# Kernel optimization log

Measured on AMD Instinct MI355X. Metric: run time of the kernel, lower is better.

## Reference

```python
import jax, jax.numpy as jnp
import numpy as np

EPS = 1e-12  # F.normalize default eps


def _l2norm(x):
    n = jnp.linalg.norm(x, axis=-1, keepdims=True)
    return x / jnp.maximum(n, EPS)


def setup_inputs() -> dict:
    key = jax.random.key(0)
    k1, k2, k3, k4 = jax.random.split(key, 4)
    N, Tq, Ts, S, D = 16, 1369, 5476, 4, 768
    return {
        "x_query": jax.random.normal(k1, (N, Tq, D), dtype=jnp.float32),
        "x_support": jax.random.normal(k2, (N, Ts, D), dtype=jnp.float32),
        "x_support_cls": jax.random.normal(k3, (N, S, D), dtype=jnp.float32),
        "W_head": jax.random.normal(k4, (3 * D, 1), dtype=jnp.float32) * 0.02,
        "b_head": jnp.zeros((1,), dtype=jnp.float32),
    }


def reference(x_query, x_support, x_support_cls, W_head, b_head):
    N, Tq, D = x_query.shape
    side = int(np.sqrt(Tq))  # token grid side, 37 for 1369 tokens

    # mean CLS over shots, then L2-normalize everything
    cls = _l2norm(jnp.mean(x_support_cls, axis=1, keepdims=True))  # [N,1,D]
    q = _l2norm(x_query)     # [N,Tq,D]
    s = _l2norm(x_support)   # [N,Ts,D]

    # cosine distance matrix and nearest-support reduction
    cd = 1.0 - jnp.einsum("nqd,nsd->nqs", q, s)      # [N,Tq,Ts]
    dmin = jnp.min(cd, axis=-1)                        # [N,Tq]
    idx = jnp.argmin(cd, axis=-1)                      # [N,Tq]
    nearest = jnp.take_along_axis(s, idx[..., None], axis=1)  # [N,Tq,D]

    # head on concat([q, nearest, cls]) -> sigmoid
    feat = jnp.concatenate(
        [q, nearest, jnp.broadcast_to(cls, (N, Tq, D))], axis=-1
    )  # [N,Tq,3D]
    logits = feat @ W_head + b_head                    # [N,Tq,1]
    pred = jax.nn.sigmoid(logits)

    dmin = dmin.reshape(N, 1, side, side)
    pred = pred.reshape(N, 1, side, side)
    return pred * dmin, pred
```

## Files before the change

kernel.cpp:

```cpp
#include <hip/hip_runtime.h>
#include <stdint.h>

#define NB 16
#define TQ 1369
#define TS 5476
#define DD 768

#define BM 128
#define BN 128
#define KB 24
#define RBQ 11
#define RBS 43
#define QPAD 1408
#define SPAD 5504
#define NROWS (NB * QPAD)
#define CAP 8
#define EPS_SEL 2.5e-3f

typedef float f32x4 __attribute__((ext_vector_type(4)));
typedef short short8 __attribute__((ext_vector_type(8)));
typedef unsigned short ushort;
typedef unsigned long long ull;


__device__ inline float waveReduceSum(float v) {
    #pragma unroll
    for (int m = 32; m >= 1; m >>= 1) v += __shfl_xor(v, m);
    return v;
}

__device__ inline unsigned bf16rne(float x) {
    unsigned u = __float_as_uint(x);
    return (u + 0x7FFFu + ((u >> 16) & 1u)) >> 16;
}
__device__ inline unsigned pack2(float lo, float hi) {
    return bf16rne(lo) | (bf16rne(hi) << 16);
}

__device__ inline f32x4 mfma16(short8 a, short8 b, f32x4 c) {
    return __builtin_amdgcn_mfma_f32_16x16x32_bf16(a, b, c, 0, 0, 0);
}

__device__ inline void async16(const void* g, void* l) {
    __builtin_amdgcn_global_load_lds(
        (const __attribute__((address_space(1))) unsigned*)g,
        (__attribute__((address_space(3))) unsigned*)l, 16, 0, 0);
}

__device__ inline unsigned fsort(float f) {
    unsigned u = __float_as_uint(f);
    return (u & 0x80000000u) ? ~u : (u | 0x80000000u);
}
__device__ inline float funsort(unsigned u) {
    return __uint_as_float((u & 0x80000000u) ? (u & 0x7FFFFFFFu) : ~u);
}


__global__ __launch_bounds__(256) void cls_kernel(const float* __restrict__ xc,
                                                  float* __restrict__ cls) {
    int n = blockIdx.x, tid = threadIdx.x;
    const float* base = xc + (size_t)n * 4 * DD;
    float v[3]; float ss = 0.f;
    #pragma unroll
    for (int i = 0; i < 3; i++) {
        int e = tid + i * 256;
        float a = base[e] + base[DD + e] + base[2 * DD + e] + base[3 * DD + e];
        v[i] = a * 0.25f; ss += v[i] * v[i];
    }
    ss = waveReduceSum(ss);
    __shared__ float red[4]; __shared__ float rn;
    if ((tid & 63) == 0) red[tid >> 6] = ss;
    __syncthreads();
    if (tid == 0) {
        float t = red[0] + red[1] + red[2] + red[3];
        rn = 1.0f / fmaxf(sqrtf(t), 1e-12f);
    }
    __syncthreads();
    float r = rn;
    #pragma unroll
    for (int i = 0; i < 3; i++) cls[(size_t)n * DD + tid + i * 256] = v[i] * r;
}


__global__ __launch_bounds__(256) void split_kernel(const float* __restrict__ Q,
                                                    const float* __restrict__ S,
                                                    ushort* __restrict__ Qh,
                                                    ushort* __restrict__ Sh,
                                                    float* __restrict__ rq,
                                                    float* __restrict__ rs) {
    int wid = (int)((blockIdx.x * 256u + threadIdx.x) >> 6);
    int lane = threadIdx.x & 63;
    bool isQ = wid < NB * QPAD;
    int n, row, nreal;
    if (isQ) { n = wid / QPAD; row = wid % QPAD; nreal = TQ; }
    else     { int w2 = wid - NB * QPAD; n = w2 / SPAD; row = w2 % SPAD; nreal = TS; }
    int rb = row >> 7, p = row & 127;
    size_t tbase = isQ ? (size_t)(n * RBQ + rb) * KB * 4096
                       : (size_t)(n * RBS + rb) * KB * 4096;
    ushort* outp = (isQ ? Qh : Sh) + tbase;

    if (row >= nreal) {
        uint4 z = {0u, 0u, 0u, 0u};
        for (int t = lane; t < 96; t += 64) {
            int kb = t >> 2, g = t & 3;
            *(uint4*)(outp + (size_t)kb * 4096 + g * 1024 + p * 8) = z;
        }
        return;
    }

    const float* src = isQ ? Q + ((size_t)n * TQ + row) * DD
                           : S + ((size_t)n * TS + row) * DD;
    float4 x[3]; float ss = 0.f;
    #pragma unroll
    for (int i = 0; i < 3; i++) {
        x[i] = ((const float4*)src)[lane + i * 64];
        ss += x[i].x * x[i].x + x[i].y * x[i].y + x[i].z * x[i].z + x[i].w * x[i].w;
    }
    ss = waveReduceSum(ss);
    float r = 1.0f / fmaxf(sqrtf(ss), 1e-12f);
    if (lane == 0) {
        if (isQ) rq[(size_t)n * TQ + row] = r; else rs[(size_t)n * TS + row] = r;
    }
    #pragma unroll
    for (int i = 0; i < 3; i++) {
        float ax = x[i].x * r, ay = x[i].y * r, az = x[i].z * r, aw = x[i].w * r;
        int k0 = lane * 4 + i * 256;
        int kb = k0 >> 5;
        int g  = (k0 >> 3) & 3;
        int sub = k0 & 7;
        uint2 hv;
        hv.x = pack2(ax, ay);
        hv.y = pack2(az, aw);
        *(uint2*)(outp + (size_t)kb * 4096 + g * 1024 + p * 8 + sub) = hv;
    }
}


__global__ __launch_bounds__(256, 4) void gemm_sel(const ushort* __restrict__ Qh,
                                                   const ushort* __restrict__ Sh,
                                                   float2* __restrict__ hdr,
                                                   uint2* __restrict__ cpair) {
    __shared__ __align__(16) ushort As[4096];
    __shared__ __align__(16) ushort Bs[4096];
    __shared__ ull key[128];
    __shared__ int cnt[128];
    __shared__ uint2 cand[128][CAP];

    int tid = threadIdx.x, w = tid >> 6, lane = tid & 63;
    int bx = blockIdx.x, by = blockIdx.y, n = blockIdx.z;
    int wm = w & 1, wn = w >> 1, g4 = lane >> 4, c16 = lane & 15;

    if (tid < 128) { key[tid] = 0ull; cnt[tid] = 1; }
    __syncthreads();

    const char* gsrc = (const char*)((w < 2)
        ? (Qh + (size_t)(n * RBQ + bx) * KB * 4096)
        : (Sh + (size_t)(n * RBS + by) * KB * 4096)) + wm * 4096 + lane * 16;
    char* lbase = (char*)((w < 2) ? As : Bs) + wm * 4096;

    f32x4 acc[4][4] = {};
    int aoff = g4 * 1024 + wm * 512 + c16 * 8;
    int boff = g4 * 1024 + wn * 512 + c16 * 8;

    for (int kb = 0; kb < KB; kb++) {
        #pragma unroll
        for (int j = 0; j < 4; j++)
            async16(gsrc + (size_t)kb * 8192 + j * 1024, lbase + j * 1024);
        __syncthreads();

        short8 ah[4], bh[4];
        #pragma unroll
        for (int i = 0; i < 4; i++) {
            ah[i] = *(const short8*)&As[aoff + i * 128];
            bh[i] = *(const short8*)&Bs[boff + i * 128];
        }
        #pragma unroll
        for (int mi = 0; mi < 4; mi++)
            #pragma unroll
            for (int ni = 0; ni < 4; ni++)
                acc[mi][ni] = mfma16(ah[mi], bh[ni], acc[mi][ni]);
        __syncthreads();
    }

    int colb = by * 128 + wn * 64 + c16;
    bool edge = (by == RBS - 1);

    #pragma unroll
    for (int mi = 0; mi < 4; mi++) {
        #pragma unroll
        for (int r = 0; r < 4; r++) {
            float v = -1e30f; int c = 0;
            #pragma unroll
            for (int ni = 0; ni < 4; ni++) {
                float d = acc[mi][ni][r];
                int col = colb + ni * 16;
                if ((!edge || col < TS) && d > v) { v = d; c = col; }
            }
            #pragma unroll
            for (int m = 1; m < 16; m <<= 1) {
                float ov = __shfl_xor(v, m);
                int   oc = __shfl_xor(c, m);
                if (ov > v || (ov == v && oc < c)) { v = ov; c = oc; }
            }
            if (c16 == 0) {
                int row = wm * 64 + mi * 16 + g4 * 4 + r;
                ull k = ((ull)fsort(v) << 32) | (unsigned)(8191 - c);
                atomicMax(&key[row], k);
            }
        }
    }
    __syncthreads();

    #pragma unroll
    for (int mi = 0; mi < 4; mi++) {
        #pragma unroll
        for (int r = 0; r < 4; r++) {
            int row = wm * 64 + mi * 16 + g4 * 4 + r;
            ull k = key[row];
            float mx = funsort((unsigned)(k >> 32));
            int amc = 8191 - (int)(k & 0xFFFFFFFFull);
            float thr = mx - EPS_SEL;
            #pragma unroll
            for (int ni = 0; ni < 4; ni++) {
                float d = acc[mi][ni][r];
                int col = colb + ni * 16;
                if ((!edge || col < TS) && d >= thr && col != amc) {
                    int slot = atomicAdd(&cnt[row], 1);
                    if (slot < CAP) {
                        uint2 pr; pr.x = (unsigned)col; pr.y = __float_as_uint(d);
                        cand[row][slot] = pr;
                    }
                }
            }
        }
    }
    __syncthreads();

    if (tid < 128) {
        ull k = key[tid];
        float mx = funsort((unsigned)(k >> 32));
        int amc = 8191 - (int)(k & 0xFFFFFFFFull);
        int cn = min(cnt[tid], CAP);
        size_t rowg = (size_t)n * QPAD + (size_t)bx * 128 + tid;
        size_t rec = (size_t)by * NROWS + rowg;
        hdr[rec] = make_float2(mx, __int_as_float(cn));
        uint2 a0; a0.x = (unsigned)amc; a0.y = __float_as_uint(mx);
        cpair[rec * CAP] = a0;
        for (int i = 1; i < cn; i++) cpair[rec * CAP + i] = cand[tid][i];
    }
}


__global__ __launch_bounds__(256) void merge_head(const float2* __restrict__ hdr,
                                                  const uint2* __restrict__ cpair,
                                                  const float* __restrict__ Q,
                                                  const float* __restrict__ S,
                                                  const float* __restrict__ rq,
                                                  const float* __restrict__ rs,
                                                  const float* __restrict__ cls,
                                                  const float* __restrict__ W,
                                                  const float* __restrict__ bb,
                                                  float* __restrict__ out) {
    int w = threadIdx.x >> 6, lane = threadIdx.x & 63;
    int qi = blockIdx.x * 4 + w;
    int n = qi / TQ, qr = qi - n * TQ;
    size_t rowg = (size_t)n * QPAD + qr;

    float mx_l = -1e30f; int cnt_l = 0;
    if (lane < RBS) {
        float2 h = hdr[(size_t)lane * NROWS + rowg];
        mx_l = h.x; cnt_l = __float_as_int(h.y);
    }
    float gm = mx_l;
    #pragma unroll
    for (int m = 32; m >= 1; m >>= 1) gm = fmaxf(gm, __shfl_xor(gm, m));
    float thr = gm - EPS_SEL;

    const float* qrow = Q + (size_t)qi * DD;
    float4 q4[3];
    #pragma unroll
    for (int i = 0; i < 3; i++) q4[i] = ((const float4*)qrow)[lane + i * 64];
    float rqv = rq[qi];

    float bestd = -1e30f; int bidx = 0x7FFFFFFF;

    auto recheck = [&](int sidx) {
        const float* srow = S + ((size_t)n * TS + sidx) * DD;
        float part = 0.f;
        #pragma unroll
        for (int k = 0; k < 3; k++) {
            float4 s4 = ((const float4*)srow)[lane + k * 64];
            part += q4[k].x * s4.x + q4[k].y * s4.y + q4[k].z * s4.z + q4[k].w * s4.w;
        }
        part = waveReduceSum(part);
        float dot = part * rqv * rs[(size_t)n * TS + sidx];
        if (dot > bestd || (dot == bestd && sidx < bidx)) { bestd = dot; bidx = sidx; }
    };

    ull ball = __ballot(lane < RBS && mx_l >= thr);
    while (ball) {
        int src = __ffsll((long long)ball) - 1;
        ball &= ball - 1;
        int cn = __shfl(cnt_l, src);
        size_t rec = (size_t)src * NROWS + rowg;
        for (int i = 0; i < cn; i++) {
            uint2 pr = cpair[rec * CAP + i];
            float ad = __uint_as_float(pr.y);
            if (ad >= thr) recheck((int)pr.x);
        }
    }
    if (bidx == 0x7FFFFFFF) bidx = 0;
    float dmin = 1.0f - bestd;

    const float* srow = S + ((size_t)n * TS + bidx) * DD;
    const float* clsr = cls + (size_t)n * DD;
    float rsv = rs[(size_t)n * TS + bidx];
    float aq = 0.f, as_ = 0.f, ac = 0.f;
    #pragma unroll
    for (int i = 0; i < 3; i++) {
        float4 s4 = ((const float4*)srow)[lane + i * 64];
        float4 c4 = ((const float4*)clsr)[lane + i * 64];
        float4 w0 = ((const float4*)W)[lane + i * 64];
        float4 w1 = ((const float4*)(W + DD))[lane + i * 64];
        float4 w2 = ((const float4*)(W + 2 * DD))[lane + i * 64];
        aq += q4[i].x * w0.x + q4[i].y * w0.y + q4[i].z * w0.z + q4[i].w * w0.w;
        as_ += s4.x * w1.x + s4.y * w1.y + s4.z * w1.z + s4.w * w1.w;
        ac += c4.x * w2.x + c4.y * w2.y + c4.z * w2.z + c4.w * w2.w;
    }
    float tot = waveReduceSum(aq * rqv + as_ * rsv + ac);
    if (lane == 0) {
        float logit = tot + bb[0];
        float pred = 1.0f / (1.0f + expf(-logit));
        out[qi] = pred * dmin;
        out[NB * TQ + qi] = pred;
    }
}


extern "C" void kernel_launch(void* const* d_in, const int* in_sizes, int n_in,
                              void* d_out, int out_size, void* d_ws, size_t ws_size,
                              hipStream_t stream) {
    const float* Q  = (const float*)d_in[0];
    const float* S  = (const float*)d_in[1];
    const float* XC = (const float*)d_in[2];
    const float* W  = (const float*)d_in[3];
    const float* B  = (const float*)d_in[4];
    (void)in_sizes; (void)n_in; (void)out_size;

    char* ws = (char*)d_ws;
    ushort* Qh    = (ushort*)ws;
    ushort* Sh    = (ushort*)(ws + 34603008ull);
    float*  rq    = (float*)(ws + 169869312ull);
    float*  rs    = (float*)(ws + 169956928ull);
    float*  cls   = (float*)(ws + 170307392ull);
    float2* hdr   = (float2*)(ws + 170356544ull);
    uint2*  cpair = (uint2*)(ws + 178106176ull);
    if (ws_size < 240103232ull) return;

    cls_kernel<<<NB, 256, 0, stream>>>(XC, cls);

    split_kernel<<<27648, 256, 0, stream>>>(Q, S, Qh, Sh, rq, rs);

    dim3 grid(RBQ, RBS, NB);
    gemm_sel<<<grid, 256, 0, stream>>>(Qh, Sh, hdr, cpair);

    merge_head<<<(NB * TQ) / 4, 256, 0, stream>>>(hdr, cpair, Q, S, rq, rs,
                                                  cls, W, B, (float*)d_out);
}
```

Measured before the change: 812.6 us.

## Split normalize-and-pack into separate norm and coalesced-store pack kernels

Replaces the single split kernel with two passes. The first computes per-row inverse L2 norms. The second has each thread pack 16 contiguous floats into two 16-byte bf16 stores in the tiled layout, where before each lane issued scattered 8-byte stores. The aim is better-coalesced writes to the packed operand buffers, at the cost of reading the fp32 inputs twice (about 300MB extra traffic) and one more kernel launch.

```diff
diff --git a/kernel.cpp b/kernel.cpp
--- a/kernel.cpp
+++ b/kernel.cpp
@@ -82,57 +82,65 @@
 }
 
 
-__global__ __launch_bounds__(256) void split_kernel(const float* __restrict__ Q,
-                                                    const float* __restrict__ S,
-                                                    ushort* __restrict__ Qh,
-                                                    ushort* __restrict__ Sh,
-                                                    float* __restrict__ rq,
-                                                    float* __restrict__ rs) {
-    int wid = (int)((blockIdx.x * 256u + threadIdx.x) >> 6);
+__global__ __launch_bounds__(256) void norm_kernel(const float* __restrict__ Q,
+                                                   const float* __restrict__ S,
+                                                   float* __restrict__ rq,
+                                                   float* __restrict__ rs) {
+    int wid = (int)(blockIdx.x * 4u + (threadIdx.x >> 6));
     int lane = threadIdx.x & 63;
-    bool isQ = wid < NB * QPAD;
-    int n, row, nreal;
-    if (isQ) { n = wid / QPAD; row = wid % QPAD; nreal = TQ; }
-    else     { int w2 = wid - NB * QPAD; n = w2 / SPAD; row = w2 % SPAD; nreal = TS; }
-    int rb = row >> 7, p = row & 127;
-    size_t tbase = isQ ? (size_t)(n * RBQ + rb) * KB * 4096
-                       : (size_t)(n * RBS + rb) * KB * 4096;
-    ushort* outp = (isQ ? Qh : Sh) + tbase;
+    bool isQ = wid < NB * TQ;
+    const float* src;
+    float* dst;
+    if (isQ) { src = Q + (size_t)wid * DD; dst = rq + wid; }
+    else     { int w2 = wid - NB * TQ; src = S + (size_t)w2 * DD; dst = rs + w2; }
+    float ss = 0.f;
+    #pragma unroll
+    for (int i = 0; i < 3; i++) {
+        float4 x = ((const float4*)src)[lane + i * 64];
+        ss += x.x * x.x + x.y * x.y + x.z * x.z + x.w * x.w;
+    }
+    ss = waveReduceSum(ss);
+    if (lane == 0) *dst = 1.0f / fmaxf(sqrtf(ss), 1e-12f);
+}
+
+
+__global__ __launch_bounds__(256) void pack_kernel(const float* __restrict__ Q,
+                                                   const float* __restrict__ S,
+                                                   const float* __restrict__ rq,
+                                                   const float* __restrict__ rs,
+                                                   ushort* __restrict__ Qh,
+                                                   ushort* __restrict__ Sh) {
+    int kb = blockIdx.x, by = blockIdx.y, n = blockIdx.z;
+    bool isQ = by < RBQ;
+    int rb = isQ ? by : by - RBQ;
+    int p = threadIdx.x & 127, half = threadIdx.x >> 7;
+    int row = rb * 128 + p;
+    int nreal = isQ ? TQ : TS;
+    ushort* outp = (isQ ? Qh + (size_t)(n * RBQ + rb) * KB * 4096
+                        : Sh + (size_t)(n * RBS + rb) * KB * 4096) + (size_t)kb * 4096;
+    int g0 = half * 2;
 
     if (row >= nreal) {
         uint4 z = {0u, 0u, 0u, 0u};
-        for (int t = lane; t < 96; t += 64) {
-            int kb = t >> 2, g = t & 3;
-            *(uint4*)(outp + (size_t)kb * 4096 + g * 1024 + p * 8) = z;
-        }
+        *(uint4*)(outp + g0 * 1024 + p * 8)       = z;
+        *(uint4*)(outp + (g0 + 1) * 1024 + p * 8) = z;
         return;
     }
 
-    const float* src = isQ ? Q + ((size_t)n * TQ + row) * DD
-                           : S + ((size_t)n * TS + row) * DD;
-    float4 x[3]; float ss = 0.f;
-    #pragma unroll
-    for (int i = 0; i < 3; i++) {
-        x[i] = ((const float4*)src)[lane + i * 64];
-        ss += x[i].x * x[i].x + x[i].y * x[i].y + x[i].z * x[i].z + x[i].w * x[i].w;
-    }
-    ss = waveReduceSum(ss);
-    float r = 1.0f / fmaxf(sqrtf(ss), 1e-12f);
-    if (lane == 0) {
-        if (isQ) rq[(size_t)n * TQ + row] = r; else rs[(size_t)n * TS + row] = r;
-    }
-    #pragma unroll
-    for (int i = 0; i < 3; i++) {
-        float ax = x[i].x * r, ay = x[i].y * r, az = x[i].z * r, aw = x[i].w * r;
-        int k0 = lane * 4 + i * 256;
-        int kb = k0 >> 5;
-        int g  = (k0 >> 3) & 3;
-        int sub = k0 & 7;
-        uint2 hv;
-        hv.x = pack2(ax, ay);
-        hv.y = pack2(az, aw);
-        *(uint2*)(outp + (size_t)kb * 4096 + g * 1024 + p * 8 + sub) = hv;
-    }
+    const float4* src = (const float4*)((isQ ? Q + ((size_t)n * TQ + row) * DD
+                                             : S + ((size_t)n * TS + row) * DD)
+                                        + kb * 32 + half * 16);
+    float r = isQ ? rq[n * TQ + row] : rs[n * TS + row];
+    float4 a = src[0], b = src[1], c = src[2], d = src[3];
+
+    uint4 o1, o2;
+    o1.x = pack2(a.x * r, a.y * r); o1.y = pack2(a.z * r, a.w * r);
+    o1.z = pack2(b.x * r, b.y * r); o1.w = pack2(b.z * r, b.w * r);
+    o2.x = pack2(c.x * r, c.y * r); o2.y = pack2(c.z * r, c.w * r);
+    o2.z = pack2(d.x * r, d.y * r); o2.w = pack2(d.z * r, d.w * r);
+
+    *(uint4*)(outp + g0 * 1024 + p * 8)       = o1;
+    *(uint4*)(outp + (g0 + 1) * 1024 + p * 8) = o2;
 }
 
 
@@ -359,7 +367,10 @@
 
     cls_kernel<<<NB, 256, 0, stream>>>(XC, cls);
 
-    split_kernel<<<27648, 256, 0, stream>>>(Q, S, Qh, Sh, rq, rs);
+    norm_kernel<<<27380, 256, 0, stream>>>(Q, S, rq, rs);
+
+    dim3 pgrid(KB, RBQ + RBS, NB);
+    pack_kernel<<<pgrid, 256, 0, stream>>>(Q, S, rq, rs, Qh, Sh);
 
     dim3 grid(RBQ, RBS, NB);
     gemm_sel<<<grid, 256, 0, stream>>>(Qh, Sh, hdr, cpair);
```

Measured after the change: 872.0 us. +7.3%, slower.
